# Performance work log

Measured on AMD Instinct MI355X. Metric: run time of the kernel, lower is better.

The kernel has to match this reference:

```python
import jax, jax.numpy as jnp
import numpy as np

N_NODES = 50000   # field_size == number of graph nodes
N_EDGES = 800000  # avg degree 16
VOCAB = 200000    # feature_size
EMB = 64          # embedding_size == in_dim
HID = 64          # num_hidden
SLOPE = 0.2       # leaky relu negative slope


def setup_inputs() -> dict:
    key = jax.random.key(0)
    ks = jax.random.split(key, 20)
    s = 0.05
    d = {}
    d["features"] = jax.random.randint(ks[0], (8, N_NODES), 0, VOCAB, dtype=jnp.int32)
    d["feature_values"] = jax.random.uniform(ks[1], (8, N_NODES), dtype=jnp.float32)
    d["src"] = jax.random.randint(ks[2], (N_EDGES,), 0, N_NODES, dtype=jnp.int32)
    d["dst"] = jax.random.randint(ks[3], (N_EDGES,), 0, N_NODES, dtype=jnp.int32)
    d["emb"] = jax.random.normal(ks[4], (VOCAB, EMB), jnp.float32) * s
    # layer 0: in=64 -> heads=2, out=64 (no residual)
    d["W0"]  = jax.random.normal(ks[5], (EMB, 2 * HID), jnp.float32) * s
    d["al0"] = jax.random.normal(ks[6], (2, HID), jnp.float32) * s
    d["ar0"] = jax.random.normal(ks[7], (2, HID), jnp.float32) * s
    d["b0"]  = jnp.zeros((2 * HID,), jnp.float32)
    # layer 1: in=128 -> heads=2, out=64 (identity residual since in == heads*out)
    d["W1"]  = jax.random.normal(ks[8], (2 * HID, 2 * HID), jnp.float32) * s
    d["al1"] = jax.random.normal(ks[9], (2, HID), jnp.float32) * s
    d["ar1"] = jax.random.normal(ks[10], (2, HID), jnp.float32) * s
    d["b1"]  = jnp.zeros((2 * HID,), jnp.float32)
    # output layer: in=128 -> heads=1, out=64 (projected residual), no activation
    d["W2"]    = jax.random.normal(ks[11], (2 * HID, EMB), jnp.float32) * s
    d["al2"]   = jax.random.normal(ks[12], (1, EMB), jnp.float32) * s
    d["ar2"]   = jax.random.normal(ks[13], (1, EMB), jnp.float32) * s
    d["b2"]    = jnp.zeros((EMB,), jnp.float32)
    d["resW2"] = jax.random.normal(ks[14], (2 * HID, EMB), jnp.float32) * s
    return d


def _gat_layer(h, src, dst, W, al, ar, b, res, act):
    """DGL-style GATConv. h: [N, in], W: [in, H*D], al/ar: [H, D]."""
    N = h.shape[0]
    H, D = al.shape
    fh = (h @ W).reshape(N, H, D)                      # [N, H, D]
    el = jnp.einsum('nhd,hd->nh', fh, al)              # [N, H]
    er = jnp.einsum('nhd,hd->nh', fh, ar)              # [N, H]
    e = jax.nn.leaky_relu(el[src] + er[dst], SLOPE)    # [E, H]
    # edge softmax grouped by destination node
    m = jax.ops.segment_max(e, dst, num_segments=N)
    m = jnp.where(jnp.isfinite(m), m, 0.0)
    ex = jnp.exp(e - m[dst])
    den = jax.ops.segment_sum(ex, dst, num_segments=N)
    alpha = ex / jnp.maximum(den[dst], 1e-9)           # [E, H]
    out = jax.ops.segment_sum(alpha[:, :, None] * fh[src], dst, num_segments=N)  # [N, H, D]
    if res is not None:
        out = out + res
    out = out + b.reshape(H, D)
    if act:
        out = jax.nn.elu(out)
    return out


def reference(features, feature_values, src, dst, emb,
              W0, al0, ar0, b0, W1, al1, ar1, b1,
              W2, al2, ar2, b2, resW2):
    # embedding lookup scaled by feature values: [B, field, emb]
    fe = emb[features] * feature_values[..., None]
    h = fe[0]                                          # [N_NODES, EMB]
    # layer 0: no residual, elu, flatten heads
    h = _gat_layer(h, src, dst, W0, al0, ar0, b0, None, True).reshape(N_NODES, -1)
    # layer 1: identity residual (in == heads*out), elu, flatten heads
    res1 = h.reshape(N_NODES, 2, HID)
    h = _gat_layer(h, src, dst, W1, al1, ar1, b1, res1, True).reshape(N_NODES, -1)
    # output layer: projected residual, no activation, mean over heads
    res2 = (h @ resW2).reshape(N_NODES, 1, EMB)
    logits = _gat_layer(h, src, dst, W2, al2, ar2, b2, res2, False).mean(axis=1)
    return logits
```

## Files before the change

### kernel.cpp

```cpp
#include <hip/hip_runtime.h>
#include <hip/hip_fp16.h>


typedef __attribute__((ext_vector_type(8))) short short8;
typedef __attribute__((ext_vector_type(4))) float float4v;

__device__ __forceinline__ float lrelu(float x){ return fmaxf(x, 0.2f*x); }

__device__ __forceinline__ unsigned short f2bf(float f){
  unsigned int u = __float_as_uint(f);
  u += 0x7fffu + ((u >> 16) & 1u);
  return (unsigned short)(u >> 16);
}
__device__ __forceinline__ unsigned short f2h(float f){
  return __half_as_ushort(__float2half(f));
}
__device__ __forceinline__ float elu1(float x){
  return x > 0.f ? x : (__expf(x) - 1.f);
}

__global__ void k_hist_rank(const int* __restrict__ dst, int* __restrict__ counts,
                            int* __restrict__ rank, int E){
  int i = blockIdx.x*blockDim.x + threadIdx.x;
  if (i < E){
    int d = dst[i];
    rank[i] = atomicAdd(&counts[d], 1);
  }
}

__global__ void k_scan_local(const int* __restrict__ counts, int* __restrict__ row_ptr,
                             int* __restrict__ bsum, int N){
  __shared__ int s[256];
  int t = threadIdx.x, g = blockIdx.x*256 + t;
  int v = (g < N) ? counts[g] : 0;
  s[t] = v; __syncthreads();
  #pragma unroll
  for (int off = 1; off < 256; off <<= 1){
    int x = 0;
    if (t >= off) x = s[t-off];
    __syncthreads();
    s[t] += x;
    __syncthreads();
  }
  if (g < N) row_ptr[g+1] = s[t];
  if (g == 0 && t == 0) row_ptr[0] = 0;
  if (t == 255) bsum[blockIdx.x] = s[255];
}

__global__ void k_scan_top(int* __restrict__ bsum, int nb){
  __shared__ int s[256];
  int t = threadIdx.x;
  int v = (t < nb) ? bsum[t] : 0;
  s[t] = v; __syncthreads();
  #pragma unroll
  for (int off = 1; off < 256; off <<= 1){
    int x = 0;
    if (t >= off) x = s[t-off];
    __syncthreads();
    s[t] += x;
    __syncthreads();
  }
  if (t < nb) bsum[t] = s[t] - v;
}

__global__ void k_scan_fix(int* __restrict__ row_ptr, const int* __restrict__ bsum, int N){
  int g = blockIdx.x*256 + threadIdx.x;
  if (g < N && blockIdx.x > 0) row_ptr[g+1] += bsum[blockIdx.x];
}

__global__ void k_scatter2(const int* __restrict__ src, const int* __restrict__ dst,
                           const int* __restrict__ rank, const int* __restrict__ row_ptr,
                           int* __restrict__ ssrc, int E){
  int i = blockIdx.x*blockDim.x + threadIdx.x;
  if (i < E) ssrc[row_ptr[dst[i]] + rank[i]] = src[i];
}

__global__ void k_setup(int* __restrict__ counts, int N,
                        const float* __restrict__ W0, const float* __restrict__ W1,
                        const float* __restrict__ W2, const float* __restrict__ rW2,
                        unsigned short* __restrict__ Wt0, unsigned short* __restrict__ Wt1,
                        unsigned short* __restrict__ Wt2){
  int id = blockIdx.x*256 + threadIdx.x;
  if (id < N){ counts[id] = 0; return; }
  int j = id - N;
  if (j < 128*64){
    int n = j/64, k = j%64;
    Wt0[n*64 + k] = f2bf(W0[k*128 + n]);
  } else if (j < 128*64 + 128*128){
    int i = j - 128*64; int n = i/128, k = i%128;
    Wt1[n*128 + k] = f2bf(W1[k*128 + n]);
  } else if (j < 128*64 + 2*128*128){
    int i = j - 128*64 - 128*128; int n = i/128, k = i%128;
    float v = (n < 64) ? W2[k*64 + n] : rW2[k*64 + (n - 64)];
    Wt2[n*128 + k] = f2bf(v);
  }
}

template<int IN, int H, bool EMBED>
__global__ __launch_bounds__(256) void k_gemm_mfma(
    const unsigned short* __restrict__ hb,
    const int* __restrict__ feat, const float* __restrict__ fv,
    const float* __restrict__ embp,
    const unsigned short* __restrict__ Wt,
    const float* __restrict__ al, const float* __restrict__ ar,
    unsigned short* __restrict__ fhb,
    float* __restrict__ elr, int N){
  constexpr int KS = IN/32;
  constexpr int LDP = IN + 8;
  __shared__ unsigned short Wt_s[128*LDP];
  const int t = threadIdx.x;
  const int lane = t & 63, wid = t >> 6;
  const int l15 = lane & 15, quad = lane >> 4;
  const int row0 = blockIdx.x*64 + wid*16;

  for (int id = t; id < 128*(IN/8); id += 256){
    int r = id/(IN/8), seg = id%(IN/8);
    ((uint4*)(Wt_s + r*LDP))[seg] = ((const uint4*)(Wt + (size_t)r*IN))[seg];
  }
  short8 a[KS];
  int arow = row0 + l15;
  if (EMBED){
    if (arow < N){
      const float* er2 = embp + (size_t)feat[arow]*64;
      float sc = fv[arow];
      #pragma unroll
      for (int s = 0; s < KS; s++){
        const float4* p = (const float4*)(er2 + s*32 + quad*8);
        float4 v0 = p[0], v1 = p[1];
        short8 ta;
        ta[0] = (short)f2bf(v0.x*sc); ta[1] = (short)f2bf(v0.y*sc);
        ta[2] = (short)f2bf(v0.z*sc); ta[3] = (short)f2bf(v0.w*sc);
        ta[4] = (short)f2bf(v1.x*sc); ta[5] = (short)f2bf(v1.y*sc);
        ta[6] = (short)f2bf(v1.z*sc); ta[7] = (short)f2bf(v1.w*sc);
        a[s] = ta;
      }
    } else {
      #pragma unroll
      for (int s = 0; s < KS; s++) a[s] = short8{0,0,0,0,0,0,0,0};
    }
  } else {
    #pragma unroll
    for (int s = 0; s < KS; s++){
      if (arow < N) a[s] = *(const short8*)(hb + (size_t)arow*IN + s*32 + quad*8);
      else          a[s] = short8{0,0,0,0,0,0,0,0};
    }
  }
  __syncthreads();

  float4v acc[8];
  #pragma unroll
  for (int nt = 0; nt < 8; nt++) acc[nt] = float4v{0.f,0.f,0.f,0.f};
  #pragma unroll
  for (int nt = 0; nt < 8; nt++){
    #pragma unroll
    for (int s = 0; s < KS; s++){
      short8 b = *(const short8*)(Wt_s + (nt*16 + l15)*LDP + s*32 + quad*8);
      acc[nt] = __builtin_amdgcn_mfma_f32_16x16x32_bf16(a[s], b, acc[nt], 0, 0, 0);
    }
  }

  float alc[8], arc[8];
  #pragma unroll
  for (int nt = 0; nt < 8; nt++){
    bool hv = (H == 2) || (nt < 4);
    alc[nt] = hv ? al[nt*16 + l15] : 0.f;
    arc[nt] = hv ? ar[nt*16 + l15] : 0.f;
  }
  #pragma unroll
  for (int reg = 0; reg < 4; reg++){
    int row = row0 + quad*4 + reg;
    bool rv = row < N;
    if (rv){
      #pragma unroll
      for (int nt = 0; nt < 8; nt++)
        fhb[(size_t)row*128 + nt*16 + l15] = f2h(acc[nt][reg]);
    }
    float pel0 = 0.f, per0 = 0.f, pel1 = 0.f, per1 = 0.f;
    #pragma unroll
    for (int nt = 0; nt < 4; nt++){
      pel0 += acc[nt][reg]*alc[nt];     per0 += acc[nt][reg]*arc[nt];
      pel1 += acc[nt+4][reg]*alc[nt+4]; per1 += acc[nt+4][reg]*arc[nt+4];
    }
    #pragma unroll
    for (int off = 1; off < 16; off <<= 1){
      pel0 += __shfl_xor(pel0, off, 64);
      pel1 += __shfl_xor(pel1, off, 64);
      per0 += __shfl_xor(per0, off, 64);
      per1 += __shfl_xor(per1, off, 64);
    }
    if (l15 == 0 && rv){
      elr[row*4+0] = pel0;
      elr[row*4+1] = (H == 2) ? pel1 : 0.f;
      elr[row*4+2] = per0;
      elr[row*4+3] = (H == 2) ? per1 : 0.f;
    }
  }
}

template<int H>
__global__ __launch_bounds__(256) void k_agg_gp(
    const unsigned short* __restrict__ fhb,
    const float* __restrict__ elr,
    const int* __restrict__ row_ptr, const int* __restrict__ ssrc,
    const float* __restrict__ bias, const float* __restrict__ res,
    int act, int res_from_fh,
    float* __restrict__ out, int out_ld, unsigned* __restrict__ outb, int N){
  const int t = threadIdx.x;
  const int gq = t >> 4, c = t & 15;
  const int n = blockIdx.x*16 + gq;
  if (n >= N) return;
  const int beg = row_ptr[n], end = row_ptr[n+1];
  const float er0 = elr[n*4+2];
  const float er1 = (H == 2) ? elr[n*4+3] : 0.f;

  const char* fhbB = (const char*)fhb;
  const unsigned cb = (H == 2) ? ((unsigned)c << 4) : ((unsigned)c << 3);
  constexpr int PC = (H == 2) ? 8 : 4;

  float acc[PC];
  #pragma unroll
  for (int k = 0; k < PC; k++) acc[k] = 0.f;
  float den0 = 0.f, den1 = 0.f;

  int i = beg;
  for (; i + 3 < end; i += 4){
    int s0 = ssrc[i],   s1 = ssrc[i+1];
    int s2 = ssrc[i+2], s3 = ssrc[i+3];
    float2 el0 = *(const float2*)(elr + s0*4);
    float2 el1 = *(const float2*)(elr + s1*4);
    float2 el2 = *(const float2*)(elr + s2*4);
    float2 el3 = *(const float2*)(elr + s3*4);
    if (H == 2){
      uint4 w0 = *(const uint4*)(fhbB + (((unsigned)s0 << 8) + cb));
      uint4 w1 = *(const uint4*)(fhbB + (((unsigned)s1 << 8) + cb));
      uint4 w2 = *(const uint4*)(fhbB + (((unsigned)s2 << 8) + cb));
      uint4 w3 = *(const uint4*)(fhbB + (((unsigned)s3 << 8) + cb));
      float e00 = __expf(fminf(lrelu(el0.x + er0), 30.f));
      float e10 = __expf(fminf(lrelu(el1.x + er0), 30.f));
      float e20 = __expf(fminf(lrelu(el2.x + er0), 30.f));
      float e30 = __expf(fminf(lrelu(el3.x + er0), 30.f));
      float e01 = __expf(fminf(lrelu(el0.y + er1), 30.f));
      float e11 = __expf(fminf(lrelu(el1.y + er1), 30.f));
      float e21 = __expf(fminf(lrelu(el2.y + er1), 30.f));
      float e31 = __expf(fminf(lrelu(el3.y + er1), 30.f));
      den0 += (e00 + e10) + (e20 + e30);
      den1 += (e01 + e11) + (e21 + e31);
      float a0 = (c < 8) ? e00 : e01;
      float a1 = (c < 8) ? e10 : e11;
      float a2 = (c < 8) ? e20 : e21;
      float a3 = (c < 8) ? e30 : e31;
      const __half2* h0 = (const __half2*)&w0;
      const __half2* h1 = (const __half2*)&w1;
      const __half2* h2 = (const __half2*)&w2;
      const __half2* h3 = (const __half2*)&w3;
      #pragma unroll
      for (int q = 0; q < 4; q++){
        acc[2*q]   = fmaf((float)h0[q].x, a0, acc[2*q]);
        acc[2*q+1] = fmaf((float)h0[q].y, a0, acc[2*q+1]);
        acc[2*q]   = fmaf((float)h1[q].x, a1, acc[2*q]);
        acc[2*q+1] = fmaf((float)h1[q].y, a1, acc[2*q+1]);
        acc[2*q]   = fmaf((float)h2[q].x, a2, acc[2*q]);
        acc[2*q+1] = fmaf((float)h2[q].y, a2, acc[2*q+1]);
        acc[2*q]   = fmaf((float)h3[q].x, a3, acc[2*q]);
        acc[2*q+1] = fmaf((float)h3[q].y, a3, acc[2*q+1]);
      }
    } else {
      uint2 w0 = *(const uint2*)(fhbB + (((unsigned)s0 << 8) + cb));
      uint2 w1 = *(const uint2*)(fhbB + (((unsigned)s1 << 8) + cb));
      uint2 w2 = *(const uint2*)(fhbB + (((unsigned)s2 << 8) + cb));
      uint2 w3 = *(const uint2*)(fhbB + (((unsigned)s3 << 8) + cb));
      float e00 = __expf(fminf(lrelu(el0.x + er0), 30.f));
      float e10 = __expf(fminf(lrelu(el1.x + er0), 30.f));
      float e20 = __expf(fminf(lrelu(el2.x + er0), 30.f));
      float e30 = __expf(fminf(lrelu(el3.x + er0), 30.f));
      den0 += (e00 + e10) + (e20 + e30);
      const __half2* h0 = (const __half2*)&w0;
      const __half2* h1 = (const __half2*)&w1;
      const __half2* h2 = (const __half2*)&w2;
      const __half2* h3 = (const __half2*)&w3;
      #pragma unroll
      for (int q = 0; q < 2; q++){
        acc[2*q]   = fmaf((float)h0[q].x, e00, acc[2*q]);
        acc[2*q+1] = fmaf((float)h0[q].y, e00, acc[2*q+1]);
        acc[2*q]   = fmaf((float)h1[q].x, e10, acc[2*q]);
        acc[2*q+1] = fmaf((float)h1[q].y, e10, acc[2*q+1]);
        acc[2*q]   = fmaf((float)h2[q].x, e20, acc[2*q]);
        acc[2*q+1] = fmaf((float)h2[q].y, e20, acc[2*q+1]);
        acc[2*q]   = fmaf((float)h3[q].x, e30, acc[2*q]);
        acc[2*q+1] = fmaf((float)h3[q].y, e30, acc[2*q+1]);
      }
    }
  }
  for (; i < end; i++){
    int s0 = ssrc[i];
    float2 el0 = *(const float2*)(elr + s0*4);
    float e00 = __expf(fminf(lrelu(el0.x + er0), 30.f));
    float e01 = (H == 2) ? __expf(fminf(lrelu(el0.y + er1), 30.f)) : 0.f;
    den0 += e00; den1 += e01;
    if (H == 2){
      uint4 w0 = *(const uint4*)(fhbB + (((unsigned)s0 << 8) + cb));
      float a0 = (c < 8) ? e00 : e01;
      const __half2* h0 = (const __half2*)&w0;
      #pragma unroll
      for (int q = 0; q < 4; q++){
        acc[2*q]   = fmaf((float)h0[q].x, a0, acc[2*q]);
        acc[2*q+1] = fmaf((float)h0[q].y, a0, acc[2*q+1]);
      }
    } else {
      uint2 w0 = *(const uint2*)(fhbB + (((unsigned)s0 << 8) + cb));
      const __half2* h0 = (const __half2*)&w0;
      #pragma unroll
      for (int q = 0; q < 2; q++){
        acc[2*q]   = fmaf((float)h0[q].x, e00, acc[2*q]);
        acc[2*q+1] = fmaf((float)h0[q].y, e00, acc[2*q+1]);
      }
    }
  }

  float rd0 = den0 > 0.f ? 1.f/den0 : 0.f;
  float rd1 = (H == 2 && den1 > 0.f) ? 1.f/den1 : 0.f;

  if (H == 2){
    float rs = (c < 8) ? rd0 : rd1;
    float o[8];
    const float4* b4 = (const float4*)(bias + c*8);
    float4 ba = b4[0], bb = b4[1];
    o[0]=fmaf(acc[0],rs,ba.x); o[1]=fmaf(acc[1],rs,ba.y);
    o[2]=fmaf(acc[2],rs,ba.z); o[3]=fmaf(acc[3],rs,ba.w);
    o[4]=fmaf(acc[4],rs,bb.x); o[5]=fmaf(acc[5],rs,bb.y);
    o[6]=fmaf(acc[6],rs,bb.z); o[7]=fmaf(acc[7],rs,bb.w);
    if (res){
      const float4* r4 = (const float4*)(res + (size_t)n*128 + c*8);
      float4 ra = r4[0], rb = r4[1];
      o[0]+=ra.x; o[1]+=ra.y; o[2]+=ra.z; o[3]+=ra.w;
      o[4]+=rb.x; o[5]+=rb.y; o[6]+=rb.z; o[7]+=rb.w;
    }
    if (act){
      #pragma unroll
      for (int k = 0; k < 8; k++) o[k] = elu1(o[k]);
    }
    if (out){
      float4* o4 = (float4*)(out + (size_t)n*out_ld + c*8);
      o4[0] = make_float4(o[0], o[1], o[2], o[3]);
      o4[1] = make_float4(o[4], o[5], o[6], o[7]);
    }
    if (outb){
      uint4 ob;
      ob.x = (unsigned)f2bf(o[0]) | ((unsigned)f2bf(o[1]) << 16);
      ob.y = (unsigned)f2bf(o[2]) | ((unsigned)f2bf(o[3]) << 16);
      ob.z = (unsigned)f2bf(o[4]) | ((unsigned)f2bf(o[5]) << 16);
      ob.w = (unsigned)f2bf(o[6]) | ((unsigned)f2bf(o[7]) << 16);
      *(uint4*)(outb + (size_t)n*64 + c*4) = ob;
    }
  } else {
    float o[4];
    #pragma unroll
    for (int k = 0; k < 4; k++) o[k] = fmaf(acc[k], rd0, bias[c*4 + k]);
    if (res_from_fh){
      uint2 r = *(const uint2*)(fhbB + (size_t)n*256 + 128 + c*8);
      const __half2* rp = (const __half2*)&r;
      o[0] += (float)rp[0].x; o[1] += (float)rp[0].y;
      o[2] += (float)rp[1].x; o[3] += (float)rp[1].y;
    }
    if (act){
      #pragma unroll
      for (int k = 0; k < 4; k++) o[k] = elu1(o[k]);
    }
    *(float4*)(out + (size_t)n*out_ld + c*4) = make_float4(o[0], o[1], o[2], o[3]);
  }
}

extern "C" void kernel_launch(void* const* d_in, const int* in_sizes, int n_in,
                              void* d_out, int out_size, void* d_ws, size_t ws_size,
                              hipStream_t stream) {
  const int*   feat = (const int*)  d_in[0];
  const float* fv   = (const float*)d_in[1];
  const int*   src  = (const int*)  d_in[2];
  const int*   dst  = (const int*)  d_in[3];
  const float* emb  = (const float*)d_in[4];
  const float* W0   = (const float*)d_in[5];
  const float* al0  = (const float*)d_in[6];
  const float* ar0  = (const float*)d_in[7];
  const float* b0   = (const float*)d_in[8];
  const float* W1   = (const float*)d_in[9];
  const float* al1  = (const float*)d_in[10];
  const float* ar1  = (const float*)d_in[11];
  const float* b1   = (const float*)d_in[12];
  const float* W2   = (const float*)d_in[13];
  const float* al2  = (const float*)d_in[14];
  const float* ar2  = (const float*)d_in[15];
  const float* b2   = (const float*)d_in[16];
  const float* rW2  = (const float*)d_in[17];
  const int N = in_sizes[0] / 8;
  const int E = in_sizes[2];

  size_t off = 0;
  auto alloc = [&](size_t bytes) -> void* {
    void* p = (char*)d_ws + off;
    off = (off + bytes + 255) & ~(size_t)255;
    return p;
  };
  unsigned short* P1 = (unsigned short*)alloc((size_t)N*128*sizeof(unsigned short));
  float* P2     = (float*)alloc((size_t)N*128*sizeof(float));
  unsigned short* hb = (unsigned short*)alloc((size_t)N*128*sizeof(unsigned short));
  float* elr    = (float*)alloc((size_t)N*4*sizeof(float));
  int* row_ptr  = (int*)alloc((size_t)(N+1)*sizeof(int));
  int* counts   = (int*)alloc((size_t)N*sizeof(int));
  int* rank     = (int*)alloc((size_t)E*sizeof(int));
  int* ssrc     = (int*)alloc((size_t)E*sizeof(int));
  int* bsum     = (int*)alloc(256*sizeof(int));
  unsigned short* Wt0 = (unsigned short*)alloc((size_t)128*64*sizeof(unsigned short));
  unsigned short* Wt1 = (unsigned short*)alloc((size_t)128*128*sizeof(unsigned short));
  unsigned short* Wt2 = (unsigned short*)alloc((size_t)128*128*sizeof(unsigned short));

  int nb1 = (N + 255) / 256;
  int eb  = (E + 255) / 256;
  k_setup<<<(N + 128*64 + 2*128*128 + 255)/256, 256, 0, stream>>>(
      counts, N, W0, W1, W2, rW2, Wt0, Wt1, Wt2);
  k_hist_rank<<<eb, 256, 0, stream>>>(dst, counts, rank, E);
  k_scan_local<<<nb1, 256, 0, stream>>>(counts, row_ptr, bsum, N);
  k_scan_top<<<1, 256, 0, stream>>>(bsum, nb1);
  k_scan_fix<<<nb1, 256, 0, stream>>>(row_ptr, bsum, N);
  k_scatter2<<<eb, 256, 0, stream>>>(src, dst, rank, row_ptr, ssrc, E);

  int gt  = (N + 63)/64;
  int ngp = (N + 15)/16;
  k_gemm_mfma<64,2,true><<<gt, 256, 0, stream>>>(nullptr, feat, fv, emb,
                                                 Wt0, al0, ar0, P1, elr, N);
  k_agg_gp<2><<<ngp, 256, 0, stream>>>(P1, elr, row_ptr, ssrc, b0, nullptr,
                                       1, 0, P2, 128, (unsigned*)hb, N);
  k_gemm_mfma<128,2,false><<<gt, 256, 0, stream>>>(hb, nullptr, nullptr, nullptr,
                                                   Wt1, al1, ar1, P1, elr, N);
  k_agg_gp<2><<<ngp, 256, 0, stream>>>(P1, elr, row_ptr, ssrc, b1, P2,
                                       1, 0, nullptr, 128, (unsigned*)hb, N);
  k_gemm_mfma<128,1,false><<<gt, 256, 0, stream>>>(hb, nullptr, nullptr, nullptr,
                                                   Wt2, al2, ar2, P1, elr, N);
  k_agg_gp<1><<<ngp, 256, 0, stream>>>(P1, elr, row_ptr, ssrc, b2, nullptr,
                                       0, 1, (float*)d_out, 64, nullptr, N);
}
```

Measured before the change: 314.3 us.

## Sort destination nodes by in-degree to balance aggregation workload

Adds a degree histogram, scan and scatter pass that builds a permutation of nodes grouped by in-degree. The three aggregation kernels then process nodes in this order, so the 16-thread groups in a wavefront have similar edge counts and less lane divergence and tail imbalance. The cost is three extra small kernel launches plus an indirection load per node. Output writes also become scattered rather than contiguous, and locality over node index is lost.

```diff
diff --git a/kernel.cpp b/kernel.cpp
--- a/kernel.cpp
+++ b/kernel.cpp
@@ -75,7 +75,41 @@
   if (i < E) ssrc[row_ptr[dst[i]] + rank[i]] = src[i];
 }
 
-__global__ void k_setup(int* __restrict__ counts, int N,
+__global__ void k_deg_hist(const int* __restrict__ counts, int* __restrict__ dcnt, int N){
+  int n = blockIdx.x*256 + threadIdx.x;
+  if (n < N) atomicAdd(&dcnt[min(counts[n], 1023)], 1);
+}
+
+__global__ void k_deg_scan(const int* __restrict__ dcnt, int* __restrict__ doff){
+  __shared__ int s[256];
+  int t = threadIdx.x;
+  int v[4]; int sum = 0;
+  #pragma unroll
+  for (int q = 0; q < 4; q++){ v[q] = dcnt[t*4+q]; sum += v[q]; }
+  s[t] = sum; __syncthreads();
+  #pragma unroll
+  for (int off = 1; off < 256; off <<= 1){
+    int x = 0;
+    if (t >= off) x = s[t-off];
+    __syncthreads();
+    s[t] += x;
+    __syncthreads();
+  }
+  int base = (t == 0) ? 0 : s[t-1];
+  #pragma unroll
+  for (int q = 0; q < 4; q++){ doff[t*4+q] = base; base += v[q]; }
+}
+
+__global__ void k_deg_scatter(const int* __restrict__ counts, int* __restrict__ doff,
+                              int* __restrict__ perm, int N){
+  int n = blockIdx.x*256 + threadIdx.x;
+  if (n < N){
+    int pos = atomicAdd(&doff[min(counts[n], 1023)], 1);
+    perm[pos] = n;
+  }
+}
+
+__global__ void k_setup(int* __restrict__ counts, int* __restrict__ dcnt, int N,
                         const float* __restrict__ W0, const float* __restrict__ W1,
                         const float* __restrict__ W2, const float* __restrict__ rW2,
                         unsigned short* __restrict__ Wt0, unsigned short* __restrict__ Wt1,
@@ -83,6 +117,8 @@
   int id = blockIdx.x*256 + threadIdx.x;
   if (id < N){ counts[id] = 0; return; }
   int j = id - N;
+  if (j < 1024){ dcnt[j] = 0; return; }
+  j -= 1024;
   if (j < 128*64){
     int n = j/64, k = j%64;
     Wt0[n*64 + k] = f2bf(W0[k*128 + n]);
@@ -202,13 +238,15 @@
     const unsigned short* __restrict__ fhb,
     const float* __restrict__ elr,
     const int* __restrict__ row_ptr, const int* __restrict__ ssrc,
+    const int* __restrict__ perm,
     const float* __restrict__ bias, const float* __restrict__ res,
     int act, int res_from_fh,
     float* __restrict__ out, int out_ld, unsigned* __restrict__ outb, int N){
   const int t = threadIdx.x;
   const int gq = t >> 4, c = t & 15;
-  const int n = blockIdx.x*16 + gq;
-  if (n >= N) return;
+  const int idx = blockIdx.x*16 + gq;
+  if (idx >= N) return;
+  const int n = perm[idx];
   const int beg = row_ptr[n], end = row_ptr[n+1];
   const float er0 = elr[n*4+2];
   const float er1 = (H == 2) ? elr[n*4+3] : 0.f;
@@ -408,6 +446,9 @@
   int* counts   = (int*)alloc((size_t)N*sizeof(int));
   int* rank     = (int*)alloc((size_t)E*sizeof(int));
   int* ssrc     = (int*)alloc((size_t)E*sizeof(int));
+  int* perm     = (int*)alloc((size_t)N*sizeof(int));
+  int* dcnt     = (int*)alloc(1024*sizeof(int));
+  int* doff     = (int*)alloc(1024*sizeof(int));
   int* bsum     = (int*)alloc(256*sizeof(int));
   unsigned short* Wt0 = (unsigned short*)alloc((size_t)128*64*sizeof(unsigned short));
   unsigned short* Wt1 = (unsigned short*)alloc((size_t)128*128*sizeof(unsigned short));
@@ -415,9 +456,12 @@
 
   int nb1 = (N + 255) / 256;
   int eb  = (E + 255) / 256;
-  k_setup<<<(N + 128*64 + 2*128*128 + 255)/256, 256, 0, stream>>>(
-      counts, N, W0, W1, W2, rW2, Wt0, Wt1, Wt2);
+  k_setup<<<(N + 1024 + 128*64 + 2*128*128 + 255)/256, 256, 0, stream>>>(
+      counts, dcnt, N, W0, W1, W2, rW2, Wt0, Wt1, Wt2);
   k_hist_rank<<<eb, 256, 0, stream>>>(dst, counts, rank, E);
+  k_deg_hist<<<nb1, 256, 0, stream>>>(counts, dcnt, N);
+  k_deg_scan<<<1, 256, 0, stream>>>(dcnt, doff);
+  k_deg_scatter<<<nb1, 256, 0, stream>>>(counts, doff, perm, N);
   k_scan_local<<<nb1, 256, 0, stream>>>(counts, row_ptr, bsum, N);
   k_scan_top<<<1, 256, 0, stream>>>(bsum, nb1);
   k_scan_fix<<<nb1, 256, 0, stream>>>(row_ptr, bsum, N);
@@ -427,14 +471,14 @@
   int ngp = (N + 15)/16;
   k_gemm_mfma<64,2,true><<<gt, 256, 0, stream>>>(nullptr, feat, fv, emb,
                                                  Wt0, al0, ar0, P1, elr, N);
-  k_agg_gp<2><<<ngp, 256, 0, stream>>>(P1, elr, row_ptr, ssrc, b0, nullptr,
+  k_agg_gp<2><<<ngp, 256, 0, stream>>>(P1, elr, row_ptr, ssrc, perm, b0, nullptr,
                                        1, 0, P2, 128, (unsigned*)hb, N);
   k_gemm_mfma<128,2,false><<<gt, 256, 0, stream>>>(hb, nullptr, nullptr, nullptr,
                                                    Wt1, al1, ar1, P1, elr, N);
-  k_agg_gp<2><<<ngp, 256, 0, stream>>>(P1, elr, row_ptr, ssrc, b1, P2,
+  k_agg_gp<2><<<ngp, 256, 0, stream>>>(P1, elr, row_ptr, ssrc, perm, b1, P2,
                                        1, 0, nullptr, 128, (unsigned*)hb, N);
   k_gemm_mfma<128,1,false><<<gt, 256, 0, stream>>>(hb, nullptr, nullptr, nullptr,
                                                    Wt2, al2, ar2, P1, elr, N);
-  k_agg_gp<1><<<ngp, 256, 0, stream>>>(P1, elr, row_ptr, ssrc, b2, nullptr,
+  k_agg_gp<1><<<ngp, 256, 0, stream>>>(P1, elr, row_ptr, ssrc, perm, b2, nullptr,
                                        0, 1, (float*)d_out, 64, nullptr, N);
 }
```

After: 580.4 us. 84.7% more time.

## Fuse aggregation with next-layer GEMM and histogram with first GEMM, switch to fp16

Applied to the files above, without the earlier changes.

Each aggregation kernel now keeps its 16 output node rows in shared memory and runs the next layer's projection GEMM (with MFMA f16) directly, writing fh and el/er for the following layer. This removes the separate GEMM launches and the bf16 round-trip of hidden activations through global memory. The edge histogram is merged into the layer-0 GEMM launch as extra blocks, and all matrix inputs move from bf16 to fp16. In exchange, weights are read from global memory per block rather than staged in LDS, el/er are reduced with shared-memory atomics, and ping-pong buffers are used.

```diff
diff --git a/kernel.cpp b/kernel.cpp
--- a/kernel.cpp
+++ b/kernel.cpp
@@ -2,30 +2,16 @@
 #include <hip/hip_fp16.h>
 
 
-typedef __attribute__((ext_vector_type(8))) short short8;
+typedef __attribute__((ext_vector_type(8))) _Float16 half8;
 typedef __attribute__((ext_vector_type(4))) float float4v;
 
 __device__ __forceinline__ float lrelu(float x){ return fmaxf(x, 0.2f*x); }
 
-__device__ __forceinline__ unsigned short f2bf(float f){
-  unsigned int u = __float_as_uint(f);
-  u += 0x7fffu + ((u >> 16) & 1u);
-  return (unsigned short)(u >> 16);
-}
 __device__ __forceinline__ unsigned short f2h(float f){
   return __half_as_ushort(__float2half(f));
 }
 __device__ __forceinline__ float elu1(float x){
   return x > 0.f ? x : (__expf(x) - 1.f);
-}
-
-__global__ void k_hist_rank(const int* __restrict__ dst, int* __restrict__ counts,
-                            int* __restrict__ rank, int E){
-  int i = blockIdx.x*blockDim.x + threadIdx.x;
-  if (i < E){
-    int d = dst[i];
-    rank[i] = atomicAdd(&counts[d], 1);
-  }
 }
 
 __global__ void k_scan_local(const int* __restrict__ counts, int* __restrict__ row_ptr,
@@ -85,29 +71,35 @@
   int j = id - N;
   if (j < 128*64){
     int n = j/64, k = j%64;
-    Wt0[n*64 + k] = f2bf(W0[k*128 + n]);
+    Wt0[n*64 + k] = f2h(W0[k*128 + n]);
   } else if (j < 128*64 + 128*128){
     int i = j - 128*64; int n = i/128, k = i%128;
-    Wt1[n*128 + k] = f2bf(W1[k*128 + n]);
+    Wt1[n*128 + k] = f2h(W1[k*128 + n]);
   } else if (j < 128*64 + 2*128*128){
     int i = j - 128*64 - 128*128; int n = i/128, k = i%128;
     float v = (n < 64) ? W2[k*64 + n] : rW2[k*64 + (n - 64)];
-    Wt2[n*128 + k] = f2bf(v);
-  }
-}
-
-template<int IN, int H, bool EMBED>
-__global__ __launch_bounds__(256) void k_gemm_mfma(
-    const unsigned short* __restrict__ hb,
+    Wt2[n*128 + k] = f2h(v);
+  }
+}
+
+__global__ __launch_bounds__(256) void k_gemm0_hist(
     const int* __restrict__ feat, const float* __restrict__ fv,
     const float* __restrict__ embp,
     const unsigned short* __restrict__ Wt,
     const float* __restrict__ al, const float* __restrict__ ar,
-    unsigned short* __restrict__ fhb,
-    float* __restrict__ elr, int N){
-  constexpr int KS = IN/32;
-  constexpr int LDP = IN + 8;
+    unsigned short* __restrict__ fhb, float* __restrict__ elr, int N, int gt,
+    const int* __restrict__ dst, int* __restrict__ counts,
+    int* __restrict__ rank, int E){
+  constexpr int IN = 64, KS = IN/32, LDP = IN + 8;
   __shared__ unsigned short Wt_s[128*LDP];
+  if ((int)blockIdx.x >= gt){
+    int i = ((int)blockIdx.x - gt)*256 + threadIdx.x;
+    if (i < E){
+      int d = dst[i];
+      rank[i] = atomicAdd(&counts[d], 1);
+    }
+    return;
+  }
   const int t = threadIdx.x;
   const int lane = t & 63, wid = t >> 6;
   const int l15 = lane & 15, quad = lane >> 4;
@@ -117,54 +109,45 @@
     int r = id/(IN/8), seg = id%(IN/8);
     ((uint4*)(Wt_s + r*LDP))[seg] = ((const uint4*)(Wt + (size_t)r*IN))[seg];
   }
-  short8 a[KS];
+  half8 a[KS];
   int arow = row0 + l15;
-  if (EMBED){
-    if (arow < N){
-      const float* er2 = embp + (size_t)feat[arow]*64;
-      float sc = fv[arow];
-      #pragma unroll
-      for (int s = 0; s < KS; s++){
-        const float4* p = (const float4*)(er2 + s*32 + quad*8);
-        float4 v0 = p[0], v1 = p[1];
-        short8 ta;
-        ta[0] = (short)f2bf(v0.x*sc); ta[1] = (short)f2bf(v0.y*sc);
-        ta[2] = (short)f2bf(v0.z*sc); ta[3] = (short)f2bf(v0.w*sc);
-        ta[4] = (short)f2bf(v1.x*sc); ta[5] = (short)f2bf(v1.y*sc);
-        ta[6] = (short)f2bf(v1.z*sc); ta[7] = (short)f2bf(v1.w*sc);
-        a[s] = ta;
-      }
-    } else {
-      #pragma unroll
-      for (int s = 0; s < KS; s++) a[s] = short8{0,0,0,0,0,0,0,0};
+  if (arow < N){
+    const float* er2 = embp + (size_t)feat[arow]*64;
+    float sc = fv[arow];
+    #pragma unroll
+    for (int s = 0; s < KS; s++){
+      const float4* p = (const float4*)(er2 + s*32 + quad*8);
+      float4 v0 = p[0], v1 = p[1];
+      half8 ta;
+      ta[0] = (_Float16)(v0.x*sc); ta[1] = (_Float16)(v0.y*sc);
+      ta[2] = (_Float16)(v0.z*sc); ta[3] = (_Float16)(v0.w*sc);
+      ta[4] = (_Float16)(v1.x*sc); ta[5] = (_Float16)(v1.y*sc);
+      ta[6] = (_Float16)(v1.z*sc); ta[7] = (_Float16)(v1.w*sc);
+      a[s] = ta;
     }
   } else {
     #pragma unroll
+    for (int s = 0; s < KS; s++) a[s] = half8{0,0,0,0,0,0,0,0};
+  }
+  __syncthreads();
+
+  float4v acc[8];
+  #pragma unroll
+  for (int nt = 0; nt < 8; nt++) acc[nt] = float4v{0.f,0.f,0.f,0.f};
+  #pragma unroll
+  for (int nt = 0; nt < 8; nt++){
+    #pragma unroll
     for (int s = 0; s < KS; s++){
-      if (arow < N) a[s] = *(const short8*)(hb + (size_t)arow*IN + s*32 + quad*8);
-      else          a[s] = short8{0,0,0,0,0,0,0,0};
-    }
-  }
-  __syncthreads();
-
-  float4v acc[8];
-  #pragma unroll
-  for (int nt = 0; nt < 8; nt++) acc[nt] = float4v{0.f,0.f,0.f,0.f};
+      half8 b = *(const half8*)(Wt_s + (nt*16 + l15)*LDP + s*32 + quad*8);
+      acc[nt] = __builtin_amdgcn_mfma_f32_16x16x32_f16(a[s], b, acc[nt], 0, 0, 0);
+    }
+  }
+
+  float alc[8], arc[8];
   #pragma unroll
   for (int nt = 0; nt < 8; nt++){
-    #pragma unroll
-    for (int s = 0; s < KS; s++){
-      short8 b = *(const short8*)(Wt_s + (nt*16 + l15)*LDP + s*32 + quad*8);
-      acc[nt] = __builtin_amdgcn_mfma_f32_16x16x32_bf16(a[s], b, acc[nt], 0, 0, 0);
-    }
-  }
-
-  float alc[8], arc[8];
-  #pragma unroll
-  for (int nt = 0; nt < 8; nt++){
-    bool hv = (H == 2) || (nt < 4);
-    alc[nt] = hv ? al[nt*16 + l15] : 0.f;
-    arc[nt] = hv ? ar[nt*16 + l15] : 0.f;
+    alc[nt] = al[nt*16 + l15];
+    arc[nt] = ar[nt*16 + l15];
   }
   #pragma unroll
   for (int reg = 0; reg < 4; reg++){
@@ -190,36 +173,44 @@
     }
     if (l15 == 0 && rv){
       elr[row*4+0] = pel0;
-      elr[row*4+1] = (H == 2) ? pel1 : 0.f;
+      elr[row*4+1] = pel1;
       elr[row*4+2] = per0;
-      elr[row*4+3] = (H == 2) ? per1 : 0.f;
-    }
-  }
-}
-
-template<int H>
-__global__ __launch_bounds__(256) void k_agg_gp(
+      elr[row*4+3] = per1;
+    }
+  }
+}
+
+template<int HN>
+__global__ __launch_bounds__(256) void k_agg_gemm(
     const unsigned short* __restrict__ fhb,
     const float* __restrict__ elr,
     const int* __restrict__ row_ptr, const int* __restrict__ ssrc,
     const float* __restrict__ bias, const float* __restrict__ res,
-    int act, int res_from_fh,
-    float* __restrict__ out, int out_ld, unsigned* __restrict__ outb, int N){
+    float* __restrict__ out,
+    const unsigned short* __restrict__ Wtn,
+    const float* __restrict__ aln, const float* __restrict__ arn,
+    unsigned short* __restrict__ fhb_out, float* __restrict__ elr_out, int N){
+  __shared__ _Float16 h_s[16*136];
+  __shared__ float elr_s[16*4];
   const int t = threadIdx.x;
   const int gq = t >> 4, c = t & 15;
-  const int n = blockIdx.x*16 + gq;
-  if (n >= N) return;
-  const int beg = row_ptr[n], end = row_ptr[n+1];
-  const float er0 = elr[n*4+2];
-  const float er1 = (H == 2) ? elr[n*4+3] : 0.f;
-
+  const int n0 = blockIdx.x*16;
+  const int n = n0 + gq;
+  const bool nv = n < N;
+  if (t < 64) elr_s[t] = 0.f;
+
+  int beg = 0, end = 0;
+  float er0 = 0.f, er1 = 0.f;
+  if (nv){
+    beg = row_ptr[n]; end = row_ptr[n+1];
+    er0 = elr[n*4+2]; er1 = elr[n*4+3];
+  }
   const char* fhbB = (const char*)fhb;
-  const unsigned cb = (H == 2) ? ((unsigned)c << 4) : ((unsigned)c << 3);
-  constexpr int PC = (H == 2) ? 8 : 4;
-
-  float acc[PC];
-  #pragma unroll
-  for (int k = 0; k < PC; k++) acc[k] = 0.f;
+  const unsigned cb = (unsigned)c << 4;
+
+  float acc[8];
+  #pragma unroll
+  for (int k = 0; k < 8; k++) acc[k] = 0.f;
   float den0 = 0.f, den1 = 0.f;
 
   int i = beg;
@@ -230,97 +221,61 @@
     float2 el1 = *(const float2*)(elr + s1*4);
     float2 el2 = *(const float2*)(elr + s2*4);
     float2 el3 = *(const float2*)(elr + s3*4);
-    if (H == 2){
-      uint4 w0 = *(const uint4*)(fhbB + (((unsigned)s0 << 8) + cb));
-      uint4 w1 = *(const uint4*)(fhbB + (((unsigned)s1 << 8) + cb));
-      uint4 w2 = *(const uint4*)(fhbB + (((unsigned)s2 << 8) + cb));
-      uint4 w3 = *(const uint4*)(fhbB + (((unsigned)s3 << 8) + cb));
-      float e00 = __expf(fminf(lrelu(el0.x + er0), 30.f));
-      float e10 = __expf(fminf(lrelu(el1.x + er0), 30.f));
-      float e20 = __expf(fminf(lrelu(el2.x + er0), 30.f));
-      float e30 = __expf(fminf(lrelu(el3.x + er0), 30.f));
-      float e01 = __expf(fminf(lrelu(el0.y + er1), 30.f));
-      float e11 = __expf(fminf(lrelu(el1.y + er1), 30.f));
-      float e21 = __expf(fminf(lrelu(el2.y + er1), 30.f));
-      float e31 = __expf(fminf(lrelu(el3.y + er1), 30.f));
-      den0 += (e00 + e10) + (e20 + e30);
-      den1 += (e01 + e11) + (e21 + e31);
-      float a0 = (c < 8) ? e00 : e01;
-      float a1 = (c < 8) ? e10 : e11;
-      float a2 = (c < 8) ? e20 : e21;
-      float a3 = (c < 8) ? e30 : e31;
-      const __half2* h0 = (const __half2*)&w0;
-      const __half2* h1 = (const __half2*)&w1;
-      const __half2* h2 = (const __half2*)&w2;
-      const __half2* h3 = (const __half2*)&w3;
-      #pragma unroll
-      for (int q = 0; q < 4; q++){
-        acc[2*q]   = fmaf((float)h0[q].x, a0, acc[2*q]);
-        acc[2*q+1] = fmaf((float)h0[q].y, a0, acc[2*q+1]);
-        acc[2*q]   = fmaf((float)h1[q].x, a1, acc[2*q]);
-        acc[2*q+1] = fmaf((float)h1[q].y, a1, acc[2*q+1]);
-        acc[2*q]   = fmaf((float)h2[q].x, a2, acc[2*q]);
-        acc[2*q+1] = fmaf((float)h2[q].y, a2, acc[2*q+1]);
-        acc[2*q]   = fmaf((float)h3[q].x, a3, acc[2*q]);
-        acc[2*q+1] = fmaf((float)h3[q].y, a3, acc[2*q+1]);
-      }
-    } else {
-      uint2 w0 = *(const uint2*)(fhbB + (((unsigned)s0 << 8) + cb));
-      uint2 w1 = *(const uint2*)(fhbB + (((unsigned)s1 << 8) + cb));
-      uint2 w2 = *(const uint2*)(fhbB + (((unsigned)s2 << 8) + cb));
-      uint2 w3 = *(const uint2*)(fhbB + (((unsigned)s3 << 8) + cb));
-      float e00 = __expf(fminf(lrelu(el0.x + er0), 30.f));
-      float e10 = __expf(fminf(lrelu(el1.x + er0), 30.f));
-      float e20 = __expf(fminf(lrelu(el2.x + er0), 30.f));
-      float e30 = __expf(fminf(lrelu(el3.x + er0), 30.f));
-      den0 += (e00 + e10) + (e20 + e30);
-      const __half2* h0 = (const __half2*)&w0;
-      const __half2* h1 = (const __half2*)&w1;
-      const __half2* h2 = (const __half2*)&w2;
-      const __half2* h3 = (const __half2*)&w3;
-      #pragma unroll
-      for (int q = 0; q < 2; q++){
-        acc[2*q]   = fmaf((float)h0[q].x, e00, acc[2*q]);
-        acc[2*q+1] = fmaf((float)h0[q].y, e00, acc[2*q+1]);
-        acc[2*q]   = fmaf((float)h1[q].x, e10, acc[2*q]);
-        acc[2*q+1] = fmaf((float)h1[q].y, e10, acc[2*q+1]);
-        acc[2*q]   = fmaf((float)h2[q].x, e20, acc[2*q]);
-        acc[2*q+1] = fmaf((float)h2[q].y, e20, acc[2*q+1]);
-        acc[2*q]   = fmaf((float)h3[q].x, e30, acc[2*q]);
-        acc[2*q+1] = fmaf((float)h3[q].y, e30, acc[2*q+1]);
-      }
+    uint4 w0 = *(const uint4*)(fhbB + (((unsigned)s0 << 8) + cb));
+    uint4 w1 = *(const uint4*)(fhbB + (((unsigned)s1 << 8) + cb));
+    uint4 w2 = *(const uint4*)(fhbB + (((unsigned)s2 << 8) + cb));
+    uint4 w3 = *(const uint4*)(fhbB + (((unsigned)s3 << 8) + cb));
+    float e00 = __expf(fminf(lrelu(el0.x + er0), 30.f));
+    float e10 = __expf(fminf(lrelu(el1.x + er0), 30.f));
+    float e20 = __expf(fminf(lrelu(el2.x + er0), 30.f));
+    float e30 = __expf(fminf(lrelu(el3.x + er0), 30.f));
+    float e01 = __expf(fminf(lrelu(el0.y + er1), 30.f));
+    float e11 = __expf(fminf(lrelu(el1.y + er1), 30.f));
+    float e21 = __expf(fminf(lrelu(el2.y + er1), 30.f));
+    float e31 = __expf(fminf(lrelu(el3.y + er1), 30.f));
+    den0 += (e00 + e10) + (e20 + e30);
+    den1 += (e01 + e11) + (e21 + e31);
+    float a0 = (c < 8) ? e00 : e01;
+    float a1 = (c < 8) ? e10 : e11;
+    float a2 = (c < 8) ? e20 : e21;
+    float a3 = (c < 8) ? e30 : e31;
+    const __half2* h0 = (const __half2*)&w0;
+    const __half2* h1 = (const __half2*)&w1;
+    const __half2* h2 = (const __half2*)&w2;
+    const __half2* h3 = (const __half2*)&w3;
+    #pragma unroll
+    for (int q = 0; q < 4; q++){
+      acc[2*q]   = fmaf((float)h0[q].x, a0, acc[2*q]);
+      acc[2*q+1] = fmaf((float)h0[q].y, a0, acc[2*q+1]);
+      acc[2*q]   = fmaf((float)h1[q].x, a1, acc[2*q]);
+      acc[2*q+1] = fmaf((float)h1[q].y, a1, acc[2*q+1]);
+      acc[2*q]   = fmaf((float)h2[q].x, a2, acc[2*q]);
+      acc[2*q+1] = fmaf((float)h2[q].y, a2, acc[2*q+1]);
+      acc[2*q]   = fmaf((float)h3[q].x, a3, acc[2*q]);
+      acc[2*q+1] = fmaf((float)h3[q].y, a3, acc[2*q+1]);
     }
   }
   for (; i < end; i++){
     int s0 = ssrc[i];
     float2 el0 = *(const float2*)(elr + s0*4);
     float e00 = __expf(fminf(lrelu(el0.x + er0), 30.f));
-    float e01 = (H == 2) ? __expf(fminf(lrelu(el0.y + er1), 30.f)) : 0.f;
+    float e01 = __expf(fminf(lrelu(el0.y + er1), 30.f));
     den0 += e00; den1 += e01;
-    if (H == 2){
-      uint4 w0 = *(const uint4*)(fhbB + (((unsigned)s0 << 8) + cb));
-      float a0 = (c < 8) ? e00 : e01;
-      const __half2* h0 = (const __half2*)&w0;
-      #pragma unroll
-      for (int q = 0; q < 4; q++){
-        acc[2*q]   = fmaf((float)h0[q].x, a0, acc[2*q]);
-        acc[2*q+1] = fmaf((float)h0[q].y, a0, acc[2*q+1]);
-      }
-    } else {
-      uint2 w0 = *(const uint2*)(fhbB + (((unsigned)s0 << 8) + cb));
-      const __half2* h0 = (const __half2*)&w0;
-      #pragma unroll
-      for (int q = 0; q < 2; q++){
-        acc[2*q]   = fmaf((float)h0[q].x, e00, acc[2*q]);
-        acc[2*q+1] = fmaf((float)h0[q].y, e00, acc[2*q+1]);
-      }
+    uint4 w0 = *(const uint4*)(fhbB + (((unsigned)s0 << 8) + cb));
+    float a0 = (c < 8) ? e00 : e01;
+    const __half2* h0 = (const __half2*)&w0;
+    #pragma unroll
+    for (int q = 0; q < 4; q++){
+      acc[2*q]   = fmaf((float)h0[q].x, a0, acc[2*q]);
+      acc[2*q+1] = fmaf((float)h0[q].y, a0, acc[2*q+1]);
     }
   }
 
   float rd0 = den0 > 0.f ? 1.f/den0 : 0.f;
-  float rd1 = (H == 2 && den1 > 0.f) ? 1.f/den1 : 0.f;
-
-  if (H == 2){
+  float rd1 = den1 > 0.f ? 1.f/den1 : 0.f;
+
+  uint4 hv = make_uint4(0,0,0,0);
+  if (nv){
     float rs = (c < 8) ? rd0 : rd1;
     float o[8];
     const float4* b4 = (const float4*)(bias + c*8);
@@ -335,39 +290,148 @@
       o[0]+=ra.x; o[1]+=ra.y; o[2]+=ra.z; o[3]+=ra.w;
       o[4]+=rb.x; o[5]+=rb.y; o[6]+=rb.z; o[7]+=rb.w;
     }
-    if (act){
-      #pragma unroll
-      for (int k = 0; k < 8; k++) o[k] = elu1(o[k]);
-    }
+    #pragma unroll
+    for (int k = 0; k < 8; k++) o[k] = elu1(o[k]);
     if (out){
-      float4* o4 = (float4*)(out + (size_t)n*out_ld + c*8);
+      float4* o4 = (float4*)(out + (size_t)n*128 + c*8);
       o4[0] = make_float4(o[0], o[1], o[2], o[3]);
       o4[1] = make_float4(o[4], o[5], o[6], o[7]);
     }
-    if (outb){
-      uint4 ob;
-      ob.x = (unsigned)f2bf(o[0]) | ((unsigned)f2bf(o[1]) << 16);
-      ob.y = (unsigned)f2bf(o[2]) | ((unsigned)f2bf(o[3]) << 16);
-      ob.z = (unsigned)f2bf(o[4]) | ((unsigned)f2bf(o[5]) << 16);
-      ob.w = (unsigned)f2bf(o[6]) | ((unsigned)f2bf(o[7]) << 16);
-      *(uint4*)(outb + (size_t)n*64 + c*4) = ob;
-    }
-  } else {
-    float o[4];
-    #pragma unroll
-    for (int k = 0; k < 4; k++) o[k] = fmaf(acc[k], rd0, bias[c*4 + k]);
-    if (res_from_fh){
-      uint2 r = *(const uint2*)(fhbB + (size_t)n*256 + 128 + c*8);
-      const __half2* rp = (const __half2*)&r;
-      o[0] += (float)rp[0].x; o[1] += (float)rp[0].y;
-      o[2] += (float)rp[1].x; o[3] += (float)rp[1].y;
-    }
-    if (act){
-      #pragma unroll
-      for (int k = 0; k < 4; k++) o[k] = elu1(o[k]);
-    }
-    *(float4*)(out + (size_t)n*out_ld + c*4) = make_float4(o[0], o[1], o[2], o[3]);
-  }
+    hv.x = (unsigned)f2h(o[0]) | ((unsigned)f2h(o[1]) << 16);
+    hv.y = (unsigned)f2h(o[2]) | ((unsigned)f2h(o[3]) << 16);
+    hv.z = (unsigned)f2h(o[4]) | ((unsigned)f2h(o[5]) << 16);
+    hv.w = (unsigned)f2h(o[6]) | ((unsigned)f2h(o[7]) << 16);
+  }
+  *(uint4*)((char*)h_s + gq*272 + c*16) = hv;
+  __syncthreads();
+
+  const int lane = t & 63, wid = t >> 6;
+  const int l15 = lane & 15, quad = lane >> 4;
+  const int head = wid >> 1;
+
+  half8 a[4];
+  #pragma unroll
+  for (int s = 0; s < 4; s++)
+    a[s] = *(const half8*)((const char*)h_s + l15*272 + s*64 + quad*16);
+
+  const int col0 = wid*32 + l15;
+  const int col1 = col0 + 16;
+  float4v ac0 = float4v{0.f,0.f,0.f,0.f}, ac1 = float4v{0.f,0.f,0.f,0.f};
+  #pragma unroll
+  for (int s = 0; s < 4; s++){
+    half8 b0 = *(const half8*)(Wtn + (size_t)col0*128 + s*32 + quad*8);
+    half8 b1 = *(const half8*)(Wtn + (size_t)col1*128 + s*32 + quad*8);
+    ac0 = __builtin_amdgcn_mfma_f32_16x16x32_f16(a[s], b0, ac0, 0, 0, 0);
+    ac1 = __builtin_amdgcn_mfma_f32_16x16x32_f16(a[s], b1, ac1, 0, 0, 0);
+  }
+
+  bool hv0 = (HN == 2) || (col0 < 64);
+  bool hv1 = (HN == 2) || (col1 < 64);
+  float al0 = hv0 ? aln[col0] : 0.f, ar0 = hv0 ? arn[col0] : 0.f;
+  float al1 = hv1 ? aln[col1] : 0.f, ar1 = hv1 ? arn[col1] : 0.f;
+
+  #pragma unroll
+  for (int reg = 0; reg < 4; reg++){
+    int nd = quad*4 + reg;
+    int row = n0 + nd;
+    if (row < N){
+      fhb_out[(size_t)row*128 + col0] = f2h(ac0[reg]);
+      fhb_out[(size_t)row*128 + col1] = f2h(ac1[reg]);
+    }
+    float pel = ac0[reg]*al0 + ac1[reg]*al1;
+    float per = ac0[reg]*ar0 + ac1[reg]*ar1;
+    #pragma unroll
+    for (int off = 1; off < 16; off <<= 1){
+      pel += __shfl_xor(pel, off, 64);
+      per += __shfl_xor(per, off, 64);
+    }
+    if (l15 == 0){
+      atomicAdd(&elr_s[nd*4 + head], pel);
+      atomicAdd(&elr_s[nd*4 + 2 + head], per);
+    }
+  }
+  __syncthreads();
+  if (t < 64){
+    int nd = t >> 2, comp = t & 3;
+    int row = n0 + nd;
+    if (row < N) elr_out[row*4 + comp] = elr_s[t];
+  }
+}
+
+__global__ __launch_bounds__(256) void k_agg_fin(
+    const unsigned short* __restrict__ fhb,
+    const float* __restrict__ elr,
+    const int* __restrict__ row_ptr, const int* __restrict__ ssrc,
+    const float* __restrict__ bias,
+    float* __restrict__ out, int N){
+  const int t = threadIdx.x;
+  const int gq = t >> 4, c = t & 15;
+  const int n = blockIdx.x*16 + gq;
+  if (n >= N) return;
+  const int beg = row_ptr[n], end = row_ptr[n+1];
+  const float er0 = elr[n*4+2];
+
+  const char* fhbB = (const char*)fhb;
+  const unsigned cb = (unsigned)c << 3;
+
+  float acc[4];
+  #pragma unroll
+  for (int k = 0; k < 4; k++) acc[k] = 0.f;
+  float den0 = 0.f;
+
+  int i = beg;
+  for (; i + 3 < end; i += 4){
+    int s0 = ssrc[i],   s1 = ssrc[i+1];
+    int s2 = ssrc[i+2], s3 = ssrc[i+3];
+    float el0 = elr[s0*4], el1 = elr[s1*4];
+    float el2 = elr[s2*4], el3 = elr[s3*4];
+    uint2 w0 = *(const uint2*)(fhbB + (((unsigned)s0 << 8) + cb));
+    uint2 w1 = *(const uint2*)(fhbB + (((unsigned)s1 << 8) + cb));
+    uint2 w2 = *(const uint2*)(fhbB + (((unsigned)s2 << 8) + cb));
+    uint2 w3 = *(const uint2*)(fhbB + (((unsigned)s3 << 8) + cb));
+    float e00 = __expf(fminf(lrelu(el0 + er0), 30.f));
+    float e10 = __expf(fminf(lrelu(el1 + er0), 30.f));
+    float e20 = __expf(fminf(lrelu(el2 + er0), 30.f));
+    float e30 = __expf(fminf(lrelu(el3 + er0), 30.f));
+    den0 += (e00 + e10) + (e20 + e30);
+    const __half2* h0 = (const __half2*)&w0;
+    const __half2* h1 = (const __half2*)&w1;
+    const __half2* h2 = (const __half2*)&w2;
+    const __half2* h3 = (const __half2*)&w3;
+    #pragma unroll
+    for (int q = 0; q < 2; q++){
+      acc[2*q]   = fmaf((float)h0[q].x, e00, acc[2*q]);
+      acc[2*q+1] = fmaf((float)h0[q].y, e00, acc[2*q+1]);
+      acc[2*q]   = fmaf((float)h1[q].x, e10, acc[2*q]);
+      acc[2*q+1] = fmaf((float)h1[q].y, e10, acc[2*q+1]);
+      acc[2*q]   = fmaf((float)h2[q].x, e20, acc[2*q]);
+      acc[2*q+1] = fmaf((float)h2[q].y, e20, acc[2*q+1]);
+      acc[2*q]   = fmaf((float)h3[q].x, e30, acc[2*q]);
+      acc[2*q+1] = fmaf((float)h3[q].y, e30, acc[2*q+1]);
+    }
+  }
+  for (; i < end; i++){
+    int s0 = ssrc[i];
+    float e00 = __expf(fminf(lrelu(elr[s0*4] + er0), 30.f));
+    den0 += e00;
+    uint2 w0 = *(const uint2*)(fhbB + (((unsigned)s0 << 8) + cb));
+    const __half2* h0 = (const __half2*)&w0;
+    #pragma unroll
+    for (int q = 0; q < 2; q++){
+      acc[2*q]   = fmaf((float)h0[q].x, e00, acc[2*q]);
+      acc[2*q+1] = fmaf((float)h0[q].y, e00, acc[2*q+1]);
+    }
+  }
+
+  float rd0 = den0 > 0.f ? 1.f/den0 : 0.f;
+  float o[4];
+  #pragma unroll
+  for (int k = 0; k < 4; k++) o[k] = fmaf(acc[k], rd0, bias[c*4 + k]);
+  uint2 r = *(const uint2*)(fhbB + (size_t)n*256 + 128 + c*8);
+  const __half2* rp = (const __half2*)&r;
+  o[0] += (float)rp[0].x; o[1] += (float)rp[0].y;
+  o[2] += (float)rp[1].x; o[3] += (float)rp[1].y;
+  *(float4*)(out + (size_t)n*64 + c*4) = make_float4(o[0], o[1], o[2], o[3]);
 }
 
 extern "C" void kernel_launch(void* const* d_in, const int* in_sizes, int n_in,
@@ -400,10 +464,11 @@
     off = (off + bytes + 255) & ~(size_t)255;
     return p;
   };
-  unsigned short* P1 = (unsigned short*)alloc((size_t)N*128*sizeof(unsigned short));
+  unsigned short* FA = (unsigned short*)alloc((size_t)N*128*sizeof(unsigned short));
+  unsigned short* FB = (unsigned short*)alloc((size_t)N*128*sizeof(unsigned short));
+  float* EA     = (float*)alloc((size_t)N*4*sizeof(float));
+  float* EB     = (float*)alloc((size_t)N*4*sizeof(float));
   float* P2     = (float*)alloc((size_t)N*128*sizeof(float));
-  unsigned short* hb = (unsigned short*)alloc((size_t)N*128*sizeof(unsigned short));
-  float* elr    = (float*)alloc((size_t)N*4*sizeof(float));
   int* row_ptr  = (int*)alloc((size_t)(N+1)*sizeof(int));
   int* counts   = (int*)alloc((size_t)N*sizeof(int));
   int* rank     = (int*)alloc((size_t)E*sizeof(int));
@@ -415,26 +480,23 @@
 
   int nb1 = (N + 255) / 256;
   int eb  = (E + 255) / 256;
+  int gt  = (N + 63)/64;
+  int ngp = (N + 15)/16;
+
   k_setup<<<(N + 128*64 + 2*128*128 + 255)/256, 256, 0, stream>>>(
       counts, N, W0, W1, W2, rW2, Wt0, Wt1, Wt2);
-  k_hist_rank<<<eb, 256, 0, stream>>>(dst, counts, rank, E);
+  k_gemm0_hist<<<gt + eb, 256, 0, stream>>>(feat, fv, emb, Wt0, al0, ar0,
+                                            FA, EA, N, gt,
+                                            dst, counts, rank, E);
   k_scan_local<<<nb1, 256, 0, stream>>>(counts, row_ptr, bsum, N);
   k_scan_top<<<1, 256, 0, stream>>>(bsum, nb1);
   k_scan_fix<<<nb1, 256, 0, stream>>>(row_ptr, bsum, N);
   k_scatter2<<<eb, 256, 0, stream>>>(src, dst, rank, row_ptr, ssrc, E);
 
-  int gt  = (N + 63)/64;
-  int ngp = (N + 15)/16;
-  k_gemm_mfma<64,2,true><<<gt, 256, 0, stream>>>(nullptr, feat, fv, emb,
-                                                 Wt0, al0, ar0, P1, elr, N);
-  k_agg_gp<2><<<ngp, 256, 0, stream>>>(P1, elr, row_ptr, ssrc, b0, nullptr,
-                                       1, 0, P2, 128, (unsigned*)hb, N);
-  k_gemm_mfma<128,2,false><<<gt, 256, 0, stream>>>(hb, nullptr, nullptr, nullptr,
-                                                   Wt1, al1, ar1, P1, elr, N);
-  k_agg_gp<2><<<ngp, 256, 0, stream>>>(P1, elr, row_ptr, ssrc, b1, P2,
-                                       1, 0, nullptr, 128, (unsigned*)hb, N);
-  k_gemm_mfma<128,1,false><<<gt, 256, 0, stream>>>(hb, nullptr, nullptr, nullptr,
-                                                   Wt2, al2, ar2, P1, elr, N);
-  k_agg_gp<1><<<ngp, 256, 0, stream>>>(P1, elr, row_ptr, ssrc, b2, nullptr,
-                                       0, 1, (float*)d_out, 64, nullptr, N);
-}
+  k_agg_gemm<2><<<ngp, 256, 0, stream>>>(FA, EA, row_ptr, ssrc, b0, nullptr,
+                                         P2, Wt1, al1, ar1, FB, EB, N);
+  k_agg_gemm<1><<<ngp, 256, 0, stream>>>(FB, EB, row_ptr, ssrc, b1, P2,
+                                         nullptr, Wt2, al2, ar2, FA, EA, N);
+  k_agg_fin<<<ngp, 256, 0, stream>>>(FA, EA, row_ptr, ssrc, b2,
+                                     (float*)d_out, N);
+}
```

After: 320.1 us. About the same (+1.8%).
